# Kernel tuning notes

Measured on AMD Instinct MI355X. Metric: run time of the kernel, lower is better.

The kernel has to match this reference:

```python
import jax, jax.numpy as jnp
import numpy as np

B, V, J, NB = 1024, 3889, 33, 10
P = (J - 1) * 9  # 288 pose-blendshape basis


def setup_inputs() -> dict:
    key = jax.random.key(0)
    ks = jax.random.split(key, 9)
    n = lambda k, s, sc=1.0: jax.random.normal(k, s, dtype=jnp.float32) * sc
    betas = n(ks[0], (B, NB))
    global_orient = n(ks[1], (B, 3), 0.5)
    body_pose = n(ks[2], (B, (J - 1) * 3), 0.3)
    transl = n(ks[3], (B, 3))
    v_template = n(ks[4], (V, 3))
    shapedirs = n(ks[5], (V, 3, NB), 0.01)
    posedirs = n(ks[6], (P, V * 3), 0.01)
    jr = jax.random.uniform(ks[7], (J, V), dtype=jnp.float32)
    J_regressor = jr / jnp.sum(jr, axis=1, keepdims=True)  # rows sum to 1
    w = jax.random.uniform(ks[8], (V, J), dtype=jnp.float32)
    lbs_weights = w / jnp.sum(w, axis=1, keepdims=True)
    # kinematic tree: chain, parents[i] < i; root parent handled specially
    parents = np.maximum(np.arange(J) - 1, 0).astype(np.int64)
    return {"betas": betas, "global_orient": global_orient, "body_pose": body_pose,
            "transl": transl, "v_template": v_template, "shapedirs": shapedirs,
            "posedirs": posedirs, "J_regressor": J_regressor,
            "lbs_weights": lbs_weights, "parents": parents}


def _rodrigues(rot_vecs):
    """Axis-angle [.., 3] -> rotation matrices [.., 3, 3] (Rodrigues)."""
    angle = jnp.linalg.norm(rot_vecs + 1e-8, axis=-1, keepdims=True)
    axis = rot_vecs / angle
    rx, ry, rz = axis[..., 0], axis[..., 1], axis[..., 2]
    z = jnp.zeros_like(rx)
    K = jnp.stack([z, -rz, ry, rz, z, -rx, -ry, rx, z], axis=-1)
    K = K.reshape(rot_vecs.shape[:-1] + (3, 3))
    s = jnp.sin(angle)[..., None]
    c = jnp.cos(angle)[..., None]
    return jnp.eye(3, dtype=rot_vecs.dtype) + s * K + (1.0 - c) * (K @ K)


def _lbs(betas, global_orient, body_pose, transl, v_template, shapedirs,
         posedirs, J_regressor, lbs_weights, parents):
    Bn = betas.shape[0]
    par = np.asarray(parents)  # static kinematic tree
    Jn = par.shape[0]
    # shape blendshapes
    v_shaped = v_template[None] + jnp.einsum('bl,vcl->bvc', betas, shapedirs)
    joints = jnp.einsum('jv,bvc->bjc', J_regressor, v_shaped)  # [B,J,3]
    # pose -> rotation matrices
    full_pose = jnp.concatenate([global_orient, body_pose], axis=1).reshape(Bn, Jn, 3)
    rot = _rodrigues(full_pose)  # [B,J,3,3]
    # pose blendshapes (identity-subtracted, root excluded)
    pose_feat = (rot[:, 1:] - jnp.eye(3, dtype=rot.dtype)).reshape(Bn, -1)  # [B,288]
    v_posed = v_shaped + (pose_feat @ posedirs).reshape(Bn, -1, 3)
    # forward kinematics: compose 4x4 transforms along the tree
    rel = joints.at[:, 1:].add(-joints[:, par[1:]])  # relative joint locations
    Tmat = jnp.concatenate([rot, rel[..., None]], axis=-1)  # [B,J,3,4]
    bottom = jnp.broadcast_to(jnp.array([0., 0., 0., 1.], Tmat.dtype), (Bn, Jn, 1, 4))
    Tmat = jnp.concatenate([Tmat, bottom], axis=2)  # [B,J,4,4]
    chain = [Tmat[:, 0]]
    for i in range(1, Jn):  # fixed small loop over joints
        chain.append(chain[int(par[i])] @ Tmat[:, i])
    transforms = jnp.stack(chain, axis=1)  # [B,J,4,4]
    # remove rest-pose joint locations from the transforms
    jh = jnp.concatenate([joints, jnp.zeros((Bn, Jn, 1), joints.dtype)], axis=-1)[..., None]
    A = transforms - jnp.pad(transforms @ jh, ((0, 0), (0, 0), (0, 0), (3, 0)))
    # linear blend skinning
    T = jnp.einsum('vj,bjmn->bvmn', lbs_weights, A)  # [B,V,4,4]
    vh = jnp.concatenate([v_posed, jnp.ones(v_posed.shape[:-1] + (1,), v_posed.dtype)], axis=-1)
    verts = jnp.einsum('bvmn,bvn->bvm', T, vh)[..., :3]
    return verts + transl[:, None]


def reference(betas, global_orient, body_pose, transl, v_template, shapedirs,
              posedirs, J_regressor, lbs_weights, parents):
    return _lbs(betas, global_orient, body_pose, transl, v_template, shapedirs,
                posedirs, J_regressor, lbs_weights, parents)
```

## Files before the change

### kernel.cpp

```cpp
#include <hip/hip_runtime.h>
#include <math.h>

#define B_  1024
#define V_  3889
#define J_  33
#define NB_ 10
#define P_  288
#define N3  11667
#define NT_ 122
#define NPAD (NT_*96)

typedef short bf16x8 __attribute__((ext_vector_type(8)));
typedef float f32x4  __attribute__((ext_vector_type(4)));

__device__ __forceinline__ unsigned short f2bf(float f) {
  union { float f; unsigned u; } v; v.f = f;
  unsigned r = v.u + 0x7FFFu + ((v.u >> 16) & 1u);
  return (unsigned short)(r >> 16);
}
__device__ __forceinline__ float bf2f(unsigned short h) {
  union { unsigned u; float f; } v; v.u = ((unsigned)h) << 16; return v.f;
}

#define PREP_JS   33
#define PREP_CVT  399
#define PREP_NB   463

__global__ __launch_bounds__(256) void k_prep(
    const float* __restrict__ Jreg, const float* __restrict__ vt,
    const float* __restrict__ sd, const float* __restrict__ pdirs,
    const float* __restrict__ lbsw,
    float* __restrict__ JS, float* __restrict__ bj,
    unsigned short* __restrict__ pdT, unsigned short* __restrict__ wbf)
{
  __shared__ __align__(16) unsigned char su[38016];
  const int bid = blockIdx.x;
  const int t = threadIdx.x;

  if (bid < PREP_JS) {
    float* red = (float*)su;
    const int j = bid;
    if (t < 128) {
      float acc[33];
      #pragma unroll
      for (int e = 0; e < 33; ++e) acc[e] = 0.f;
      for (int v = t; v < V_; v += 128) {
        float r = Jreg[j*V_ + v];
        #pragma unroll
        for (int c = 0; c < 3; ++c) {
          acc[c*11 + 10] += r * vt[v*3 + c];
          #pragma unroll
          for (int l = 0; l < NB_; ++l)
            acc[c*11 + l] += r * sd[v*30 + c*10 + l];
        }
      }
      #pragma unroll
      for (int e = 0; e < 33; ++e) red[e*128 + t] = acc[e];
    }
    __syncthreads();
    if (t < 33) {
      float s = 0.f;
      for (int i = 0; i < 128; ++i) s += red[t*128 + i];
      int c = t / 11, l = t % 11;
      if (l == 10) bj[j*3 + c] = s;
      else         JS[(j*3 + c)*NB_ + l] = s;
    }
  } else if (bid < PREP_CVT) {
    float* tile = (float*)su;
    const int bb = bid - PREP_JS;
    const int nt = bb / 3;
    const int c0 = (bb % 3) * 32;
    for (int i = t; i < P_*32; i += 256) {
      int k = i >> 5, c = i & 31;
      int gc = nt*96 + c0 + c;
      tile[k*33 + c] = (gc < N3) ? pdirs[(size_t)k*N3 + gc] : 0.f;
    }
    __syncthreads();
    for (int o = t; o < 32*36; o += 256) {
      int c = o / 36, kg = o - 36*c;
      bf16x8 pk;
      #pragma unroll
      for (int j = 0; j < 8; ++j)
        pk[j] = (short)f2bf(tile[(kg*8 + j)*33 + c]);
      *(bf16x8*)&pdT[((size_t)(nt*96 + c0 + c))*P_ + kg*8] = pk;
    }
  } else {
    const int bb = bid - PREP_CVT;
    const int total = 4096*96;
    for (int i = bb*256 + t; i < total; i += 64*256) {
      int v = i / 96, k = i - 96*v;
      float val = 0.f;
      if (v < V_) {
        if (k < 33) val = lbsw[(size_t)v*33 + k];
        else if (k < 66) {
          float w = lbsw[(size_t)v*33 + (k-33)];
          val = w - bf2f(f2bf(w));
        }
      }
      wbf[i] = f2bf(val);
    }
  }
}

__global__ __launch_bounds__(64) void k_pose(
    const float* __restrict__ betas, const float* __restrict__ go,
    const float* __restrict__ bp, const float* __restrict__ JS,
    const float* __restrict__ bj,
    unsigned short* __restrict__ pfb,
    unsigned short* __restrict__ Abf)
{
  const int b = blockIdx.x;
  const int t = threadIdx.x;
  __shared__ float rot[J_][9];
  __shared__ float jnt[J_][3];
  __shared__ float Ash[J_][12];
  __shared__ float bsh[NB_];
  if (t < NB_) bsh[t] = betas[b*NB_ + t];
  __syncthreads();
  if (t < J_) {
    #pragma unroll
    for (int c = 0; c < 3; ++c) {
      float s = bj[t*3 + c];
      #pragma unroll
      for (int l = 0; l < NB_; ++l) s += bsh[l] * JS[(t*3 + c)*NB_ + l];
      jnt[t][c] = s;
    }
    float px, py, pz;
    if (t == 0) { px = go[b*3+0]; py = go[b*3+1]; pz = go[b*3+2]; }
    else {
      const float* p = bp + (size_t)b*((J_-1)*3) + (t-1)*3;
      px = p[0]; py = p[1]; pz = p[2];
    }
    float ax = px + 1e-8f, ay = py + 1e-8f, az = pz + 1e-8f;
    float ang = sqrtf(ax*ax + ay*ay + az*az);
    float inv = 1.0f / ang;
    float ux = px*inv, uy = py*inv, uz = pz*inv;
    float sn = sinf(ang), cs = cosf(ang);
    float K[9] = {0.f,-uz,uy,  uz,0.f,-ux,  -uy,ux,0.f};
    float R[9];
    #pragma unroll
    for (int r = 0; r < 3; ++r)
      #pragma unroll
      for (int c = 0; c < 3; ++c) {
        float k2 = K[r*3+0]*K[0*3+c] + K[r*3+1]*K[1*3+c] + K[r*3+2]*K[2*3+c];
        float id = (r == c) ? 1.f : 0.f;
        R[r*3+c] = id + sn*K[r*3+c] + (1.f - cs)*k2;
      }
    #pragma unroll
    for (int e = 0; e < 9; ++e) rot[t][e] = R[e];
    if (t >= 1) {
      #pragma unroll
      for (int e = 0; e < 9; ++e)
        pfb[(size_t)b*P_ + (t-1)*9 + e] = f2bf(R[e] - ((e==0||e==4||e==8) ? 1.f : 0.f));
    }
  }
  __syncthreads();
  if (t == 0) {
    float G[12];
    #pragma unroll
    for (int r = 0; r < 3; ++r) {
      G[r*4+0] = rot[0][r*3+0]; G[r*4+1] = rot[0][r*3+1];
      G[r*4+2] = rot[0][r*3+2]; G[r*4+3] = jnt[0][r];
    }
    for (int j = 0; j < J_; ++j) {
      if (j > 0) {
        float rel0 = jnt[j][0] - jnt[j-1][0];
        float rel1 = jnt[j][1] - jnt[j-1][1];
        float rel2 = jnt[j][2] - jnt[j-1][2];
        float N[12];
        #pragma unroll
        for (int r = 0; r < 3; ++r) {
          #pragma unroll
          for (int c = 0; c < 3; ++c)
            N[r*4+c] = G[r*4+0]*rot[j][0*3+c] + G[r*4+1]*rot[j][1*3+c] + G[r*4+2]*rot[j][2*3+c];
          N[r*4+3] = G[r*4+0]*rel0 + G[r*4+1]*rel1 + G[r*4+2]*rel2 + G[r*4+3];
        }
        #pragma unroll
        for (int e = 0; e < 12; ++e) G[e] = N[e];
      }
      #pragma unroll
      for (int r = 0; r < 3; ++r) {
        Ash[j][r*4+0] = G[r*4+0];
        Ash[j][r*4+1] = G[r*4+1];
        Ash[j][r*4+2] = G[r*4+2];
        Ash[j][r*4+3] = G[r*4+3] - (G[r*4+0]*jnt[j][0] + G[r*4+1]*jnt[j][1] + G[r*4+2]*jnt[j][2]);
      }
    }
  }
  __syncthreads();
  const float* Af = &Ash[0][0];
  for (int i = t; i < 1536; i += 64) {
    int n = i / 96, k = i - 96*n;
    int j = (k < 33) ? k : ((k < 66) ? (k - 33) : -1);
    float val = 0.f;
    if (j >= 0) {
      if (n < 12) val = Af[j*12 + n];
      else if (n < 15) {
        float tr = Af[j*12 + (n-12)*4 + 3];
        val = tr - bf2f(f2bf(tr));
      }
    }
    Abf[(size_t)b*1536 + i] = f2bf(val);
  }
}

#define TS 17

__global__ __launch_bounds__(256, 2) void k_gs(
    const float* __restrict__ betas,
    const float* __restrict__ vt, const float* __restrict__ sd,
    const unsigned short* __restrict__ pdT,
    const unsigned short* __restrict__ pfb_g,
    const float* __restrict__ transl,
    const unsigned short* __restrict__ wbf,
    const unsigned short* __restrict__ Abf,
    float* __restrict__ out)
{
  __shared__ float s_beta[640];
  __shared__ float s_tr[192];
  __shared__ float s_vp[64*100];
  __shared__ float s_T[4][2*32*TS];

  const int hw  = blockIdx.x;
  const int wg  = (hw & 7) * 244 + (hw >> 3);
  const int nt  = wg >> 4;
  const int bt  = wg & 15;
  const int b0  = bt*64;

  const int tid = threadIdx.x;
  const int lane = tid & 63, wid = tid >> 6;
  const int wm = wid >> 1, wn = wid & 1;
  const int l15 = lane & 15, lg = lane >> 4;

  for (int i = tid; i < 64*NB_; i += 256) s_beta[i] = betas[(size_t)b0*NB_ + i];
  for (int i = tid; i < 192; i += 256) s_tr[i] = transl[(size_t)b0*3 + i];

  bf16x8 afr[2][3];
  #pragma unroll
  for (int mt = 0; mt < 2; ++mt) {
    const int vrow = nt*32 + mt*16 + l15;
    #pragma unroll
    for (int ks = 0; ks < 3; ++ks)
      afr[mt][ks] = *(const bf16x8*)&wbf[(size_t)vrow*96 + ks*32 + lg*8];
  }
  __syncthreads();

  f32x4 acc[2][3];
  #pragma unroll
  for (int f = 0; f < 3; ++f) {
    int colL = wn*48 + f*16 + l15;
    int gc = nt*96 + colL;
    if (gc < N3) {
      int v = gc/3, c = gc - 3*v;
      float base = vt[gc];
      float sval[2][4];
      #pragma unroll
      for (int mi = 0; mi < 2; ++mi)
        #pragma unroll
        for (int reg = 0; reg < 4; ++reg) sval[mi][reg] = base;
      #pragma unroll
      for (int l = 0; l < NB_; ++l) {
        float sdv = sd[(size_t)v*30 + c*10 + l];
        #pragma unroll
        for (int mi = 0; mi < 2; ++mi) {
          int row_b = mi*32 + wm*16 + lg*4;
          #pragma unroll
          for (int reg = 0; reg < 4; ++reg)
            sval[mi][reg] += s_beta[(row_b+reg)*NB_ + l] * sdv;
        }
      }
      #pragma unroll
      for (int mi = 0; mi < 2; ++mi) {
        acc[mi][f][0]=sval[mi][0]; acc[mi][f][1]=sval[mi][1];
        acc[mi][f][2]=sval[mi][2]; acc[mi][f][3]=sval[mi][3];
      }
    } else {
      #pragma unroll
      for (int mi = 0; mi < 2; ++mi)
        acc[mi][f] = (f32x4){0.f,0.f,0.f,0.f};
    }
  }

  const unsigned short* __restrict__ pfrow0 =
      pfb_g + (size_t)(b0 + wm*16 + l15)*P_ + lg*8;
  const unsigned short* __restrict__ pfrow1 =
      pfb_g + (size_t)(b0 + 32 + wm*16 + l15)*P_ + lg*8;
  const unsigned short* __restrict__ pdrow =
      pdT + (size_t)(nt*96 + wn*48 + l15)*P_ + lg*8;
  __builtin_amdgcn_s_setprio(1);
  #pragma unroll
  for (int ks = 0; ks < 9; ++ks) {
    bf16x8 a0 = *(const bf16x8*)(pfrow0 + ks*32);
    bf16x8 a1 = *(const bf16x8*)(pfrow1 + ks*32);
    #pragma unroll
    for (int f = 0; f < 3; ++f) {
      bf16x8 b = *(const bf16x8*)(pdrow + (size_t)f*16*P_ + ks*32);
      acc[0][f] = __builtin_amdgcn_mfma_f32_16x16x32_bf16(a0, b, acc[0][f], 0, 0, 0);
      acc[1][f] = __builtin_amdgcn_mfma_f32_16x16x32_bf16(a1, b, acc[1][f], 0, 0, 0);
    }
  }
  __builtin_amdgcn_s_setprio(0);

  bf16x8 bcur[2][3];
  #pragma unroll
  for (int h = 0; h < 2; ++h) {
    const unsigned short* Ab = Abf + (size_t)(b0 + wid*16 + h)*1536;
    #pragma unroll
    for (int ks = 0; ks < 3; ++ks)
      bcur[h][ks] = *(const bf16x8*)&Ab[l15*96 + ks*32 + lg*8];
  }

  #pragma unroll
  for (int f = 0; f < 3; ++f) {
    int colL = wn*48 + f*16 + l15;
    #pragma unroll
    for (int mi = 0; mi < 2; ++mi) {
      int row_b = mi*32 + wm*16 + lg*4;
      #pragma unroll
      for (int reg = 0; reg < 4; ++reg)
        s_vp[(row_b+reg)*100 + colL] = acc[mi][f][reg];
    }
  }
  __syncthreads();

  float* Tw = &s_T[wid][0];
  const int h2 = lane >> 5, vl = lane & 31;
  const int v = nt*32 + vl;

  float pxc = s_vp[(wid*16 + h2)*100 + vl*3 + 0];
  float pyc = s_vp[(wid*16 + h2)*100 + vl*3 + 1];
  float pzc = s_vp[(wid*16 + h2)*100 + vl*3 + 2];

  #pragma unroll 2
  for (int g = 0; g < 8; ++g) {
    bf16x8 bnxt[2][3];
    float pxn = 0.f, pyn = 0.f, pzn = 0.f;
    if (g < 7) {
      #pragma unroll
      for (int h = 0; h < 2; ++h) {
        const unsigned short* Ab = Abf + (size_t)(b0 + wid*16 + (g+1)*2 + h)*1536;
        #pragma unroll
        for (int ks = 0; ks < 3; ++ks)
          bnxt[h][ks] = *(const bf16x8*)&Ab[l15*96 + ks*32 + lg*8];
      }
      int bln = wid*16 + (g+1)*2 + h2;
      pxn = s_vp[bln*100 + vl*3 + 0];
      pyn = s_vp[bln*100 + vl*3 + 1];
      pzn = s_vp[bln*100 + vl*3 + 2];
    }

    __builtin_amdgcn_s_setprio(1);
    #pragma unroll
    for (int h = 0; h < 2; ++h) {
      f32x4 t0 = {0.f,0.f,0.f,0.f}, t1 = t0;
      #pragma unroll
      for (int ks = 0; ks < 3; ++ks) {
        t0 = __builtin_amdgcn_mfma_f32_16x16x32_bf16(afr[0][ks], bcur[h][ks], t0, 0, 0, 0);
        t1 = __builtin_amdgcn_mfma_f32_16x16x32_bf16(afr[1][ks], bcur[h][ks], t1, 0, 0, 0);
      }
      #pragma unroll
      for (int reg = 0; reg < 4; ++reg) {
        Tw[h*32*TS + (lg*4+reg)*TS + l15]      = t0[reg];
        Tw[h*32*TS + (16+lg*4+reg)*TS + l15]   = t1[reg];
      }
    }
    __builtin_amdgcn_s_setprio(0);
    {
      const int bl2 = wid*16 + g*2 + h2;
      const int b2  = b0 + bl2;
      const float* Tr = Tw + h2*32*TS + vl*TS;
      float o0 = Tr[0]*pxc + Tr[1]*pyc + Tr[2]*pzc  + Tr[3]  + Tr[12] + s_tr[bl2*3+0];
      float o1 = Tr[4]*pxc + Tr[5]*pyc + Tr[6]*pzc  + Tr[7]  + Tr[13] + s_tr[bl2*3+1];
      float o2 = Tr[8]*pxc + Tr[9]*pyc + Tr[10]*pzc + Tr[11] + Tr[14] + s_tr[bl2*3+2];
      if (v < V_) {
        size_t po = (size_t)b2*N3 + (size_t)v*3;
        out[po+0] = o0; out[po+1] = o1; out[po+2] = o2;
      }
    }
    if (g < 7) {
      #pragma unroll
      for (int h = 0; h < 2; ++h)
        #pragma unroll
        for (int ks = 0; ks < 3; ++ks)
          bcur[h][ks] = bnxt[h][ks];
      pxc = pxn; pyc = pyn; pzc = pzn;
    }
  }
}

extern "C" void kernel_launch(void* const* d_in, const int* in_sizes, int n_in,
                              void* d_out, int out_size, void* d_ws, size_t ws_size,
                              hipStream_t stream) {
  const float* betas  = (const float*)d_in[0];
  const float* go     = (const float*)d_in[1];
  const float* bp     = (const float*)d_in[2];
  const float* transl = (const float*)d_in[3];
  const float* vt     = (const float*)d_in[4];
  const float* sd     = (const float*)d_in[5];
  const float* pdirs  = (const float*)d_in[6];
  const float* Jreg   = (const float*)d_in[7];
  const float* lbsw   = (const float*)d_in[8];
  float* out = (float*)d_out;
  char* wb = (char*)d_ws;

  float* JS            = (float*)(wb + 0);
  float* bj            = (float*)(wb + 4096);
  unsigned short* pfb  = (unsigned short*)(wb + 1630720);
  unsigned short* Abf  = (unsigned short*)(wb + 2221056);
  unsigned short* pdT  = (unsigned short*)(wb + 5366784);
  unsigned short* wbf  = (unsigned short*)(wb + 12112896);

  hipLaunchKernelGGL(k_prep, dim3(PREP_NB), dim3(256), 0, stream,
                     Jreg, vt, sd, pdirs, lbsw, JS, bj, pdT, wbf);
  hipLaunchKernelGGL(k_pose, dim3(B_), dim3(64), 0, stream,
                     betas, go, bp, JS, bj, pfb, Abf);
  hipLaunchKernelGGL(k_gs,   dim3(NT_*16), dim3(256), 0, stream,
                     betas, vt, sd, pdT, pfb, transl, wbf, Abf, out);
}
```

Before: 105.2 us.

## Regroup prep stages so pose work runs concurrently with basis conversion

The joint-shape reduction moves into its own small kernel. The per-batch pose/transform computation is merged into the same launch as the posedirs and skinning-weight bf16 conversion, so those independent stages run together instead of pose waiting for the whole prep kernel. The intent is to cut the serialized tail of the old prep kernel, where 33 heavy reduction blocks gated the pose kernel. In exchange, the pose blocks now launch with 256 threads and a large shared-memory allocation, which may lower occupancy for that work.

```diff
diff --git a/kernel.cpp b/kernel.cpp
--- a/kernel.cpp
+++ b/kernel.cpp
@@ -22,52 +22,156 @@
   union { unsigned u; float f; } v; v.u = ((unsigned)h) << 16; return v.f;
 }
 
-#define PREP_JS   33
-#define PREP_CVT  399
-#define PREP_NB   463
-
-__global__ __launch_bounds__(256) void k_prep(
+__global__ __launch_bounds__(128) void k_js(
     const float* __restrict__ Jreg, const float* __restrict__ vt,
-    const float* __restrict__ sd, const float* __restrict__ pdirs,
-    const float* __restrict__ lbsw,
-    float* __restrict__ JS, float* __restrict__ bj,
-    unsigned short* __restrict__ pdT, unsigned short* __restrict__ wbf)
+    const float* __restrict__ sd, float* __restrict__ JS, float* __restrict__ bj)
+{
+  const int j = blockIdx.x;
+  const int t = threadIdx.x;
+  float acc[33];
+  #pragma unroll
+  for (int e = 0; e < 33; ++e) acc[e] = 0.f;
+  for (int v = t; v < V_; v += 128) {
+    float r = Jreg[j*V_ + v];
+    #pragma unroll
+    for (int c = 0; c < 3; ++c) {
+      acc[c*11 + 10] += r * vt[v*3 + c];
+      #pragma unroll
+      for (int l = 0; l < NB_; ++l)
+        acc[c*11 + l] += r * sd[v*30 + c*10 + l];
+    }
+  }
+  __shared__ float red[33][128];
+  #pragma unroll
+  for (int e = 0; e < 33; ++e) red[e][t] = acc[e];
+  __syncthreads();
+  if (t < 33) {
+    float s = 0.f;
+    for (int i = 0; i < 128; ++i) s += red[t][i];
+    int c = t / 11, l = t % 11;
+    if (l == 10) bj[j*3 + c] = s;
+    else         JS[(j*3 + c)*NB_ + l] = s;
+  }
+}
+
+#define MID_POSE 1024
+#define MID_CVT  1390
+#define MID_NB   1454
+
+__global__ __launch_bounds__(256) void k_mid(
+    const float* __restrict__ betas, const float* __restrict__ go,
+    const float* __restrict__ bp, const float* __restrict__ JS,
+    const float* __restrict__ bj,
+    const float* __restrict__ vt, const float* __restrict__ sd,
+    const float* __restrict__ pdirs, const float* __restrict__ lbsw,
+    unsigned short* __restrict__ pfb,
+    unsigned short* __restrict__ Abf,
+    unsigned short* __restrict__ pdT,
+    unsigned short* __restrict__ wbf)
 {
   __shared__ __align__(16) unsigned char su[38016];
   const int bid = blockIdx.x;
   const int t = threadIdx.x;
 
-  if (bid < PREP_JS) {
-    float* red = (float*)su;
-    const int j = bid;
-    if (t < 128) {
-      float acc[33];
-      #pragma unroll
-      for (int e = 0; e < 33; ++e) acc[e] = 0.f;
-      for (int v = t; v < V_; v += 128) {
-        float r = Jreg[j*V_ + v];
+  if (bid < MID_POSE) {
+    float* rot = (float*)su;
+    float* jnt = rot + 297;
+    float* Ash = jnt + 99;
+    float* bsh = Ash + 396;
+    const int b = bid;
+    if (t < NB_) bsh[t] = betas[b*NB_ + t];
+    __syncthreads();
+    if (t < J_) {
+      #pragma unroll
+      for (int c = 0; c < 3; ++c) {
+        float s = bj[t*3 + c];
+        #pragma unroll
+        for (int l = 0; l < NB_; ++l) s += bsh[l] * JS[(t*3 + c)*NB_ + l];
+        jnt[t*3 + c] = s;
+      }
+      float px, py, pz;
+      if (t == 0) { px = go[b*3+0]; py = go[b*3+1]; pz = go[b*3+2]; }
+      else {
+        const float* p = bp + (size_t)b*((J_-1)*3) + (t-1)*3;
+        px = p[0]; py = p[1]; pz = p[2];
+      }
+      float ax = px + 1e-8f, ay = py + 1e-8f, az = pz + 1e-8f;
+      float ang = sqrtf(ax*ax + ay*ay + az*az);
+      float inv = 1.0f / ang;
+      float ux = px*inv, uy = py*inv, uz = pz*inv;
+      float sn = sinf(ang), cs = cosf(ang);
+      float K[9] = {0.f,-uz,uy,  uz,0.f,-ux,  -uy,ux,0.f};
+      float R[9];
+      #pragma unroll
+      for (int r = 0; r < 3; ++r)
         #pragma unroll
         for (int c = 0; c < 3; ++c) {
-          acc[c*11 + 10] += r * vt[v*3 + c];
+          float k2 = K[r*3+0]*K[0*3+c] + K[r*3+1]*K[1*3+c] + K[r*3+2]*K[2*3+c];
+          float id = (r == c) ? 1.f : 0.f;
+          R[r*3+c] = id + sn*K[r*3+c] + (1.f - cs)*k2;
+        }
+      #pragma unroll
+      for (int e = 0; e < 9; ++e) rot[t*9 + e] = R[e];
+      if (t >= 1) {
+        #pragma unroll
+        for (int e = 0; e < 9; ++e)
+          pfb[(size_t)b*P_ + (t-1)*9 + e] = f2bf(R[e] - ((e==0||e==4||e==8) ? 1.f : 0.f));
+      }
+    }
+    __syncthreads();
+    if (t == 0) {
+      float G[12];
+      #pragma unroll
+      for (int r = 0; r < 3; ++r) {
+        G[r*4+0] = rot[0*9 + r*3+0]; G[r*4+1] = rot[0*9 + r*3+1];
+        G[r*4+2] = rot[0*9 + r*3+2]; G[r*4+3] = jnt[0*3 + r];
+      }
+      for (int j = 0; j < J_; ++j) {
+        if (j > 0) {
+          float rel0 = jnt[j*3+0] - jnt[(j-1)*3+0];
+          float rel1 = jnt[j*3+1] - jnt[(j-1)*3+1];
+          float rel2 = jnt[j*3+2] - jnt[(j-1)*3+2];
+          float N[12];
           #pragma unroll
-          for (int l = 0; l < NB_; ++l)
-            acc[c*11 + l] += r * sd[v*30 + c*10 + l];
-        }
-      }
-      #pragma unroll
-      for (int e = 0; e < 33; ++e) red[e*128 + t] = acc[e];
+          for (int r = 0; r < 3; ++r) {
+            #pragma unroll
+            for (int c = 0; c < 3; ++c)
+              N[r*4+c] = G[r*4+0]*rot[j*9 + 0*3+c] + G[r*4+1]*rot[j*9 + 1*3+c] + G[r*4+2]*rot[j*9 + 2*3+c];
+            N[r*4+3] = G[r*4+0]*rel0 + G[r*4+1]*rel1 + G[r*4+2]*rel2 + G[r*4+3];
+          }
+          #pragma unroll
+          for (int e = 0; e < 12; ++e) G[e] = N[e];
+        }
+        #pragma unroll
+        for (int r = 0; r < 3; ++r) {
+          Ash[j*12 + r*4+0] = G[r*4+0];
+          Ash[j*12 + r*4+1] = G[r*4+1];
+          Ash[j*12 + r*4+2] = G[r*4+2];
+          Ash[j*12 + r*4+3] = G[r*4+3] -
+            (G[r*4+0]*jnt[j*3+0] + G[r*4+1]*jnt[j*3+1] + G[r*4+2]*jnt[j*3+2]);
+        }
+      }
     }
     __syncthreads();
-    if (t < 33) {
-      float s = 0.f;
-      for (int i = 0; i < 128; ++i) s += red[t*128 + i];
-      int c = t / 11, l = t % 11;
-      if (l == 10) bj[j*3 + c] = s;
-      else         JS[(j*3 + c)*NB_ + l] = s;
-    }
-  } else if (bid < PREP_CVT) {
+    if (t < 64) {
+      const float* Af = Ash;
+      for (int i = t; i < 1536; i += 64) {
+        int n = i / 96, k = i - 96*n;
+        int j = (k < 33) ? k : ((k < 66) ? (k - 33) : -1);
+        float val = 0.f;
+        if (j >= 0) {
+          if (n < 12) val = Af[j*12 + n];
+          else if (n < 15) {
+            float tr = Af[j*12 + (n-12)*4 + 3];
+            val = tr - bf2f(f2bf(tr));
+          }
+        }
+        Abf[(size_t)b*1536 + i] = f2bf(val);
+      }
+    }
+  } else if (bid < MID_CVT) {
     float* tile = (float*)su;
-    const int bb = bid - PREP_JS;
+    const int bb = bid - MID_POSE;
     const int nt = bb / 3;
     const int c0 = (bb % 3) * 32;
     for (int i = t; i < P_*32; i += 256) {
@@ -85,7 +189,7 @@
       *(bf16x8*)&pdT[((size_t)(nt*96 + c0 + c))*P_ + kg*8] = pk;
     }
   } else {
-    const int bb = bid - PREP_CVT;
+    const int bb = bid - MID_CVT;
     const int total = 4096*96;
     for (int i = bb*256 + t; i < total; i += 64*256) {
       int v = i / 96, k = i - 96*v;
@@ -99,108 +203,6 @@
       }
       wbf[i] = f2bf(val);
     }
-  }
-}
-
-__global__ __launch_bounds__(64) void k_pose(
-    const float* __restrict__ betas, const float* __restrict__ go,
-    const float* __restrict__ bp, const float* __restrict__ JS,
-    const float* __restrict__ bj,
-    unsigned short* __restrict__ pfb,
-    unsigned short* __restrict__ Abf)
-{
-  const int b = blockIdx.x;
-  const int t = threadIdx.x;
-  __shared__ float rot[J_][9];
-  __shared__ float jnt[J_][3];
-  __shared__ float Ash[J_][12];
-  __shared__ float bsh[NB_];
-  if (t < NB_) bsh[t] = betas[b*NB_ + t];
-  __syncthreads();
-  if (t < J_) {
-    #pragma unroll
-    for (int c = 0; c < 3; ++c) {
-      float s = bj[t*3 + c];
-      #pragma unroll
-      for (int l = 0; l < NB_; ++l) s += bsh[l] * JS[(t*3 + c)*NB_ + l];
-      jnt[t][c] = s;
-    }
-    float px, py, pz;
-    if (t == 0) { px = go[b*3+0]; py = go[b*3+1]; pz = go[b*3+2]; }
-    else {
-      const float* p = bp + (size_t)b*((J_-1)*3) + (t-1)*3;
-      px = p[0]; py = p[1]; pz = p[2];
-    }
-    float ax = px + 1e-8f, ay = py + 1e-8f, az = pz + 1e-8f;
-    float ang = sqrtf(ax*ax + ay*ay + az*az);
-    float inv = 1.0f / ang;
-    float ux = px*inv, uy = py*inv, uz = pz*inv;
-    float sn = sinf(ang), cs = cosf(ang);
-    float K[9] = {0.f,-uz,uy,  uz,0.f,-ux,  -uy,ux,0.f};
-    float R[9];
-    #pragma unroll
-    for (int r = 0; r < 3; ++r)
-      #pragma unroll
-      for (int c = 0; c < 3; ++c) {
-        float k2 = K[r*3+0]*K[0*3+c] + K[r*3+1]*K[1*3+c] + K[r*3+2]*K[2*3+c];
-        float id = (r == c) ? 1.f : 0.f;
-        R[r*3+c] = id + sn*K[r*3+c] + (1.f - cs)*k2;
-      }
-    #pragma unroll
-    for (int e = 0; e < 9; ++e) rot[t][e] = R[e];
-    if (t >= 1) {
-      #pragma unroll
-      for (int e = 0; e < 9; ++e)
-        pfb[(size_t)b*P_ + (t-1)*9 + e] = f2bf(R[e] - ((e==0||e==4||e==8) ? 1.f : 0.f));
-    }
-  }
-  __syncthreads();
-  if (t == 0) {
-    float G[12];
-    #pragma unroll
-    for (int r = 0; r < 3; ++r) {
-      G[r*4+0] = rot[0][r*3+0]; G[r*4+1] = rot[0][r*3+1];
-      G[r*4+2] = rot[0][r*3+2]; G[r*4+3] = jnt[0][r];
-    }
-    for (int j = 0; j < J_; ++j) {
-      if (j > 0) {
-        float rel0 = jnt[j][0] - jnt[j-1][0];
-        float rel1 = jnt[j][1] - jnt[j-1][1];
-        float rel2 = jnt[j][2] - jnt[j-1][2];
-        float N[12];
-        #pragma unroll
-        for (int r = 0; r < 3; ++r) {
-          #pragma unroll
-          for (int c = 0; c < 3; ++c)
-            N[r*4+c] = G[r*4+0]*rot[j][0*3+c] + G[r*4+1]*rot[j][1*3+c] + G[r*4+2]*rot[j][2*3+c];
-          N[r*4+3] = G[r*4+0]*rel0 + G[r*4+1]*rel1 + G[r*4+2]*rel2 + G[r*4+3];
-        }
-        #pragma unroll
-        for (int e = 0; e < 12; ++e) G[e] = N[e];
-      }
-      #pragma unroll
-      for (int r = 0; r < 3; ++r) {
-        Ash[j][r*4+0] = G[r*4+0];
-        Ash[j][r*4+1] = G[r*4+1];
-        Ash[j][r*4+2] = G[r*4+2];
-        Ash[j][r*4+3] = G[r*4+3] - (G[r*4+0]*jnt[j][0] + G[r*4+1]*jnt[j][1] + G[r*4+2]*jnt[j][2]);
-      }
-    }
-  }
-  __syncthreads();
-  const float* Af = &Ash[0][0];
-  for (int i = t; i < 1536; i += 64) {
-    int n = i / 96, k = i - 96*n;
-    int j = (k < 33) ? k : ((k < 66) ? (k - 33) : -1);
-    float val = 0.f;
-    if (j >= 0) {
-      if (n < 12) val = Af[j*12 + n];
-      else if (n < 15) {
-        float tr = Af[j*12 + (n-12)*4 + 3];
-        val = tr - bf2f(f2bf(tr));
-      }
-    }
-    Abf[(size_t)b*1536 + i] = f2bf(val);
   }
 }
 
@@ -410,10 +412,9 @@
   unsigned short* pdT  = (unsigned short*)(wb + 5366784);
   unsigned short* wbf  = (unsigned short*)(wb + 12112896);
 
-  hipLaunchKernelGGL(k_prep, dim3(PREP_NB), dim3(256), 0, stream,
-                     Jreg, vt, sd, pdirs, lbsw, JS, bj, pdT, wbf);
-  hipLaunchKernelGGL(k_pose, dim3(B_), dim3(64), 0, stream,
-                     betas, go, bp, JS, bj, pfb, Abf);
-  hipLaunchKernelGGL(k_gs,   dim3(NT_*16), dim3(256), 0, stream,
+  hipLaunchKernelGGL(k_js,  dim3(J_),     dim3(128), 0, stream, Jreg, vt, sd, JS, bj);
+  hipLaunchKernelGGL(k_mid, dim3(MID_NB), dim3(256), 0, stream,
+                     betas, go, bp, JS, bj, vt, sd, pdirs, lbsw, pfb, Abf, pdT, wbf);
+  hipLaunchKernelGGL(k_gs,  dim3(NT_*16), dim3(256), 0, stream,
                      betas, vt, sd, pdT, pfb, transl, wbf, Abf, out);
 }
```

Measured after the change: 113.2 us. 7.6% more time.
